# Optimization experiments

Measured on AMD Instinct MI355X. Metric: run time of the kernel, lower is better.

The kernel has to match this reference:

```python
import jax, jax.numpy as jnp
import numpy as np

B, L, D = 64, 4096, 256

def setup_inputs() -> dict:
    key = jax.random.key(0)
    k1, k2 = jax.random.split(key)
    inp = jax.random.normal(k1, (B, L, D), dtype=jnp.float32)
    # lengths in [1, L] so no empty-sequence mean (matches original assumption)
    length = jax.random.randint(k2, (B,), 1, L + 1, dtype=jnp.int64)
    return {"input": inp, "length": length}

def reference(input, length):
    # One fused masked mean over the ragged sequence dim.
    # mask: [B, L] True for valid positions
    mask = (jnp.arange(input.shape[1])[None, :] < length[:, None])
    m = mask.astype(input.dtype)[:, :, None]            # [B, L, 1]
    summed = jnp.sum(input * m, axis=1)                  # [B, D]
    return summed / length.astype(input.dtype)[:, None] # [B, D]
```

## Files before the change

### kernel.cpp

```cpp
#include <hip/hip_runtime.h>

#define BB 64
#define LL 4096
#define DD 256
#define D4 (DD / 4)
#define RPC 32
#define CPB 4
#define ROWS_PER_BLOCK (RPC * CPB)
#define BPB (LL / ROWS_PER_BLOCK)
#define RWAVES 8

__global__ __launch_bounds__(256) void avg_partial_kernel(
    const float* __restrict__ in,
    const int* __restrict__ len,
    float* __restrict__ ws)
{
    const int w    = threadIdx.x >> 6;
    const int lane = threadIdx.x & 63;
    const int b    = blockIdx.x / BPB;
    const int s    = blockIdx.x % BPB;

    int lb = len[b];
    if (lb < 1) lb = 1;

    if (s * ROWS_PER_BLOCK >= lb) return;

    const int row0 = s * ROWS_PER_BLOCK + w * RPC;

    float4 acc = make_float4(0.f, 0.f, 0.f, 0.f);
    if (row0 < lb) {
        int n = lb - row0;
        if (n > RPC) n = RPC;
        const float4* __restrict__ base =
            (const float4*)(in + (size_t)b * LL * DD) + (size_t)row0 * D4 + lane;
        #pragma unroll 8
        for (int r = 0; r < n; ++r) {
            float4 v = base[(size_t)r * D4];
            acc.x += v.x; acc.y += v.y; acc.z += v.z; acc.w += v.w;
        }
    }

    __shared__ float4 sh[CPB - 1][64];
    if (w > 0) sh[w - 1][lane] = acc;
    __syncthreads();

    if (w == 0) {
        #pragma unroll
        for (int i = 0; i < CPB - 1; ++i) {
            float4 v = sh[i][lane];
            acc.x += v.x; acc.y += v.y; acc.z += v.z; acc.w += v.w;
        }
        ((float4*)ws)[((size_t)b * BPB + s) * D4 + lane] = acc;
    }
}

__global__ __launch_bounds__(512) void avg_reduce_kernel(
    const float* __restrict__ ws,
    const int* __restrict__ len,
    float* __restrict__ out)
{
    const int b    = blockIdx.x;
    const int w    = threadIdx.x >> 6;
    const int lane = threadIdx.x & 63;

    int lb = len[b];
    if (lb < 1) lb = 1;
    const int nslots = (lb + ROWS_PER_BLOCK - 1) / ROWS_PER_BLOCK;

    float4 acc = make_float4(0.f, 0.f, 0.f, 0.f);
    const float4* __restrict__ wsb = (const float4*)ws + (size_t)b * BPB * D4;

    #pragma unroll 4
    for (int s = w; s < nslots; s += RWAVES) {
        float4 v = wsb[(size_t)s * D4 + lane];
        acc.x += v.x; acc.y += v.y; acc.z += v.z; acc.w += v.w;
    }

    __shared__ float4 sh[RWAVES - 1][64];
    if (w > 0) sh[w - 1][lane] = acc;
    __syncthreads();

    if (w == 0) {
        #pragma unroll
        for (int i = 0; i < RWAVES - 1; ++i) {
            float4 v = sh[i][lane];
            acc.x += v.x; acc.y += v.y; acc.z += v.z; acc.w += v.w;
        }
        const float inv = 1.0f / (float)lb;
        float4 o = make_float4(acc.x * inv, acc.y * inv, acc.z * inv, acc.w * inv);
        ((float4*)out)[(size_t)b * D4 + lane] = o;
    }
}

__global__ void avg_zero_out_kernel(float* __restrict__ out) {
    int i = blockIdx.x * blockDim.x + threadIdx.x;
    if (i < BB * DD) out[i] = 0.f;
}

__global__ __launch_bounds__(64) void avg_atomic_kernel(
    const float* __restrict__ in,
    const int* __restrict__ len,
    float* __restrict__ out)
{
    const int b    = blockIdx.x >> 6;
    const int p    = blockIdx.x & 63;
    const int lane = threadIdx.x;

    int lb = len[b];
    if (lb < 1) lb = 1;
    const int row0 = p * 64;
    int rend = row0 + 64;
    if (rend > lb) rend = (lb > row0) ? lb : row0;
    if (rend <= row0) return;

    float4 acc = make_float4(0.f, 0.f, 0.f, 0.f);
    const float4* __restrict__ base = (const float4*)(in + (size_t)b * LL * DD);
    for (int r = row0; r < rend; ++r) {
        float4 v = base[(size_t)r * D4 + lane];
        acc.x += v.x; acc.y += v.y; acc.z += v.z; acc.w += v.w;
    }
    const float inv = 1.0f / (float)lb;
    float* o = out + (size_t)b * DD + lane * 4;
    atomicAdd(o + 0, acc.x * inv);
    atomicAdd(o + 1, acc.y * inv);
    atomicAdd(o + 2, acc.z * inv);
    atomicAdd(o + 3, acc.w * inv);
}

extern "C" void kernel_launch(void* const* d_in, const int* in_sizes, int n_in,
                              void* d_out, int out_size, void* d_ws, size_t ws_size,
                              hipStream_t stream) {
    const float* in  = (const float*)d_in[0];
    const int*   len = (const int*)d_in[1];
    float*       out = (float*)d_out;

    const size_t ws_needed = (size_t)BB * BPB * DD * sizeof(float);

    if (d_ws != nullptr && ws_size >= ws_needed) {
        float* ws = (float*)d_ws;
        avg_partial_kernel<<<BB * BPB, 64 * CPB, 0, stream>>>(in, len, ws);
        avg_reduce_kernel<<<BB, 64 * RWAVES, 0, stream>>>(ws, len, out);
    } else {
        avg_zero_out_kernel<<<(BB * DD + 255) / 256, 256, 0, stream>>>(out);
        avg_atomic_kernel<<<BB * 64, 64, 0, stream>>>(in, len, out);
    }
}
```

Baseline: 28.75 us.

## Fuse partial and final reduction via last-block-done atomic counter

Merges the two-kernel partial/reduce scheme into one kernel. Each block writes its partial sum, fences, and increments a per-batch counter, and the last block to finish sums all partials and writes the mean. This removes the second kernel launch and its dependency gap but adds a hipMemsetAsync to reset the counters, plus fences and atomics. The final reduction is now serial over slots in a single wave.

Result: slower. 92.65 us (+222.3%).

```diff
diff --git a/kernel.cpp b/kernel.cpp
--- a/kernel.cpp
+++ b/kernel.cpp
@@ -8,12 +8,15 @@
 #define CPB 4
 #define ROWS_PER_BLOCK (RPC * CPB)
 #define BPB (LL / ROWS_PER_BLOCK)
-#define RWAVES 8
 
-__global__ __launch_bounds__(256) void avg_partial_kernel(
+#define WS_PART_OFF 4096
+
+__global__ __launch_bounds__(256) void avg_fused_kernel(
     const float* __restrict__ in,
     const int* __restrict__ len,
-    float* __restrict__ ws)
+    int* __restrict__ cnt,
+    float* __restrict__ part,
+    float* __restrict__ out)
 {
     const int w    = threadIdx.x >> 6;
     const int lane = threadIdx.x & 63;
@@ -22,8 +25,8 @@
 
     int lb = len[b];
     if (lb < 1) lb = 1;
-
-    if (s * ROWS_PER_BLOCK >= lb) return;
+    const int nslots = (lb + ROWS_PER_BLOCK - 1) >> 7;
+    if (s >= nslots) return;
 
     const int row0 = s * ROWS_PER_BLOCK + w * RPC;
 
@@ -43,51 +46,31 @@
     __shared__ float4 sh[CPB - 1][64];
     if (w > 0) sh[w - 1][lane] = acc;
     __syncthreads();
+    if (w != 0) return;
 
-    if (w == 0) {
-        #pragma unroll
-        for (int i = 0; i < CPB - 1; ++i) {
-            float4 v = sh[i][lane];
-            acc.x += v.x; acc.y += v.y; acc.z += v.z; acc.w += v.w;
-        }
-        ((float4*)ws)[((size_t)b * BPB + s) * D4 + lane] = acc;
-    }
-}
-
-__global__ __launch_bounds__(512) void avg_reduce_kernel(
-    const float* __restrict__ ws,
-    const int* __restrict__ len,
-    float* __restrict__ out)
-{
-    const int b    = blockIdx.x;
-    const int w    = threadIdx.x >> 6;
-    const int lane = threadIdx.x & 63;
-
-    int lb = len[b];
-    if (lb < 1) lb = 1;
-    const int nslots = (lb + ROWS_PER_BLOCK - 1) / ROWS_PER_BLOCK;
-
-    float4 acc = make_float4(0.f, 0.f, 0.f, 0.f);
-    const float4* __restrict__ wsb = (const float4*)ws + (size_t)b * BPB * D4;
-
-    #pragma unroll 4
-    for (int s = w; s < nslots; s += RWAVES) {
-        float4 v = wsb[(size_t)s * D4 + lane];
+    #pragma unroll
+    for (int i = 0; i < CPB - 1; ++i) {
+        float4 v = sh[i][lane];
         acc.x += v.x; acc.y += v.y; acc.z += v.z; acc.w += v.w;
     }
 
-    __shared__ float4 sh[RWAVES - 1][64];
-    if (w > 0) sh[w - 1][lane] = acc;
-    __syncthreads();
+    float4* __restrict__ pb = (float4*)part + (size_t)b * BPB * D4;
+    pb[(size_t)s * D4 + lane] = acc;
 
-    if (w == 0) {
-        #pragma unroll
-        for (int i = 0; i < RWAVES - 1; ++i) {
-            float4 v = sh[i][lane];
-            acc.x += v.x; acc.y += v.y; acc.z += v.z; acc.w += v.w;
+    __threadfence();
+    int old = 0;
+    if (lane == 0) old = atomicAdd(&cnt[b], 1);
+    old = __shfl(old, 0, 64);
+
+    if (old == nslots - 1) {
+        __threadfence();
+        float4 r = make_float4(0.f, 0.f, 0.f, 0.f);
+        for (int t = 0; t < nslots; ++t) {
+            float4 v = pb[(size_t)t * D4 + lane];
+            r.x += v.x; r.y += v.y; r.z += v.z; r.w += v.w;
         }
         const float inv = 1.0f / (float)lb;
-        float4 o = make_float4(acc.x * inv, acc.y * inv, acc.z * inv, acc.w * inv);
+        float4 o = make_float4(r.x * inv, r.y * inv, r.z * inv, r.w * inv);
         ((float4*)out)[(size_t)b * D4 + lane] = o;
     }
 }
@@ -134,12 +117,13 @@
     const int*   len = (const int*)d_in[1];
     float*       out = (float*)d_out;
 
-    const size_t ws_needed = (size_t)BB * BPB * DD * sizeof(float);
+    const size_t ws_needed = WS_PART_OFF + (size_t)BB * BPB * DD * sizeof(float);
 
     if (d_ws != nullptr && ws_size >= ws_needed) {
-        float* ws = (float*)d_ws;
-        avg_partial_kernel<<<BB * BPB, 64 * CPB, 0, stream>>>(in, len, ws);
-        avg_reduce_kernel<<<BB, 64 * RWAVES, 0, stream>>>(ws, len, out);
+        int*   cnt  = (int*)d_ws;
+        float* part = (float*)((char*)d_ws + WS_PART_OFF);
+        hipMemsetAsync(cnt, 0, BB * sizeof(int), stream);
+        avg_fused_kernel<<<BB * BPB, 64 * CPB, 0, stream>>>(in, len, cnt, part, out);
     } else {
         avg_zero_out_kernel<<<(BB * DD + 255) / 256, 256, 0, stream>>>(out);
         avg_atomic_kernel<<<BB * 64, 64, 0, stream>>>(in, len, out);
```
